# Performance work log

Hardware: AMD Instinct MI355X
Metric: run time of the kernel (lower is better)

The kernel has to match this reference:

```python
import jax, jax.numpy as jnp
import numpy as np
from jax import lax

WINDOW_SIZE = 11
NUM_SCALES = 4
SIGMA = 1.5
C1 = 0.01 ** 2
C2 = 0.03 ** 2
MS_WEIGHTS = (0.0448, 0.2856, 0.3001, 0.2363, 0.1333)


def _gaussian_window(window_size, sigma, channel, dtype):
    coords = jnp.arange(window_size, dtype=jnp.float32) - window_size // 2
    g = jnp.exp(-(coords ** 2) / (2.0 * sigma ** 2))
    g = g / g.sum()
    w2d = jnp.outer(g, g)  # [ws, ws]
    # depthwise kernel: [C, 1, ws, ws] (OIHW with feature_group_count=C)
    return jnp.broadcast_to(w2d, (channel, 1, window_size, window_size)).astype(dtype)


def _depthwise_conv(x, window, pad):
    C = x.shape[1]
    return lax.conv_general_dilated(
        x, window, window_strides=(1, 1), padding=[(pad, pad), (pad, pad)],
        dimension_numbers=('NCHW', 'OIHW', 'NCHW'), feature_group_count=C)


def _avg_pool2(x):
    s = lax.reduce_window(x, jnp.array(0.0, x.dtype), lax.add,
                          (1, 1, 2, 2), (1, 1, 2, 2), 'VALID')
    return s * jnp.asarray(0.25, x.dtype)


def _ssim_single_scale(img1, img2, window):
    pad = WINDOW_SIZE // 2
    mu1 = _depthwise_conv(img1, window, pad)
    mu2 = _depthwise_conv(img2, window, pad)
    mu1_sq = mu1 * mu1
    mu2_sq = mu2 * mu2
    mu1_mu2 = mu1 * mu2
    sigma1_sq = _depthwise_conv(img1 * img1, window, pad) - mu1_sq
    sigma2_sq = _depthwise_conv(img2 * img2, window, pad) - mu2_sq
    sigma12 = _depthwise_conv(img1 * img2, window, pad) - mu1_mu2
    ssim_map = ((2 * mu1_mu2 + C1) * (2 * sigma12 + C2)) / \
               ((mu1_sq + mu2_sq + C1) * (sigma1_sq + sigma2_sq + C2))
    return ssim_map.mean()  # size_average=True


def setup_inputs() -> dict:
    key = jax.random.key(0)
    k1, k2 = jax.random.split(key)
    shape = (16, 3, 512, 512)
    img1 = jax.random.uniform(k1, shape, dtype=jnp.float32)
    img2 = jax.random.uniform(k2, shape, dtype=jnp.float32)
    return {"img1": img1, "img2": img2}


def reference(img1, img2):
    channel = img1.shape[1]
    window = _gaussian_window(WINDOW_SIZE, SIGMA, channel, img1.dtype)
    loss = jnp.asarray(0.0, img1.dtype)
    x1, x2 = img1, img2
    for scale in range(NUM_SCALES):
        if scale > 0:
            x1 = _avg_pool2(x1)
            x2 = _avg_pool2(x2)
        ssim_val = _ssim_single_scale(x1, x2, window)
        w = MS_WEIGHTS[scale] if scale < len(MS_WEIGHTS) else 1.0 / NUM_SCALES
        loss = loss + w * (1.0 - ssim_val)
    return loss
```

## Files before the change

### kernel.cpp

```cpp
#include <hip/hip_runtime.h>

typedef float f2 __attribute__((ext_vector_type(2)));
typedef float f4 __attribute__((ext_vector_type(4)));

#define PAD 5
#define WSZ 11

__device__ __forceinline__ float gw(int k) {
    const float G[WSZ] = {
        0.0010283782f, 0.0075987580f, 0.0360007600f, 0.1093607000f,
        0.2130055600f, 0.2660117400f,
        0.2130055600f, 0.1093607000f, 0.0360007600f, 0.0075987580f, 0.0010283782f };
    return G[k];
}

__global__ __launch_bounds__(64) void pyramid_kernel(
    const float* __restrict__ img1, const float* __restrict__ img2,
    f2* __restrict__ p1, f2* __restrict__ p2, f2* __restrict__ p3)
{
    const int lane = threadIdx.x;
    const int cb = blockIdx.x;
    const int rb = blockIdx.y;
    const int z  = blockIdx.z;

    const size_t ibase = (size_t)z * 262144 + (size_t)(rb * 8) * 512 + cb * 256 + lane * 4;
    const float* b1 = img1 + ibase;
    const float* b2 = img2 + ibase;

    f4 A[8], B[8];
#pragma unroll
    for (int r = 0; r < 8; ++r) {
        A[r] = *(const f4*)(b1 + r * 512);
        B[r] = *(const f4*)(b2 + r * 512);
    }

    f2 u0, u1;
#pragma unroll
    for (int q = 0; q < 2; ++q) {
        f2 acc = {0.f, 0.f};
#pragma unroll
        for (int h = 0; h < 2; ++h) {
            const int rp = q * 2 + h;
            f4 a0 = A[2 * rp], a1 = A[2 * rp + 1];
            f4 c0 = B[2 * rp], c1 = B[2 * rp + 1];
            f2 v0 = { (a0.x + a0.y + a1.x + a1.y) * 0.25f,
                      (c0.x + c0.y + c1.x + c1.y) * 0.25f };
            f2 v1 = { (a0.z + a0.w + a1.z + a1.w) * 0.25f,
                      (c0.z + c0.w + c1.z + c1.w) * 0.25f };
            *(f4*)(p1 + (size_t)z * 65536 + (size_t)(rb * 4 + rp) * 256
                       + cb * 128 + lane * 2) = (f4){ v0.x, v0.y, v1.x, v1.y };
            acc += v0 + v1;
        }
        f2 u = acc * 0.25f;
        p2[(size_t)z * 16384 + (size_t)(rb * 2 + q) * 128 + cb * 64 + lane] = u;
        if (q == 0) u0 = u; else u1 = u;
    }
    f2 t = u0 + u1;
    t.x += __shfl_xor(t.x, 1);
    t.y += __shfl_xor(t.y, 1);
    if ((lane & 1) == 0)
        p3[(size_t)z * 4096 + (size_t)rb * 64 + cb * 32 + (lane >> 1)] = t * 0.25f;
}

template<int RT, bool PLANAR>
__device__ __forceinline__ float ssim_body(
    const float* __restrict__ img1, const float* __restrict__ img2,
    const f2* __restrict__ pair,
    int H, int W, int bx, int sy, int z, f2* st, int lane)
{
    const int ox = bx * 64;
    const int r0 = sy * RT;
    const size_t base = (size_t)z * H * W;

    constexpr int NIT  = RT + 10;
    constexpr int NIT2 = NIT / 2;
    const float C1 = 1e-4f, C2 = 9e-4f;

    const int c0 = ox - PAD + lane;
    const bool m0 = (c0 >= 0) & (c0 < W);
    const int c0c = min(max(c0, 0), W - 1);
    const int c1 = ox + 59 + lane;
    const bool m1 = (lane < 10) & (c1 < W);
    const int c1c = min(c1, W - 1);

    f2 P0a0={0.f,0.f}, P0a1={0.f,0.f}, P0b0={0.f,0.f}, P0b1={0.f,0.f};
    f2 P1a0={0.f,0.f}, P1a1={0.f,0.f}, P1b0={0.f,0.f}, P1b1={0.f,0.f};

    auto issue2 = [&](int y, f2& A0, f2& A1, f2& B0, f2& B1) {
        const int ya = min(max(y, 0), H - 1);
        const int yb = min(max(y + 1, 0), H - 1);
        const size_t ra = base + (size_t)ya * W;
        const size_t rb = base + (size_t)yb * W;
        if (PLANAR) {
            A0 = (f2){ img1[ra + c0c], img2[ra + c0c] };
            A1 = (f2){ img1[rb + c0c], img2[rb + c0c] };
            if (lane < 10) {
                B0 = (f2){ img1[ra + c1c], img2[ra + c1c] };
                B1 = (f2){ img1[rb + c1c], img2[rb + c1c] };
            }
        } else {
            A0 = pair[ra + c0c];
            A1 = pair[rb + c0c];
            if (lane < 10) { B0 = pair[ra + c1c]; B1 = pair[rb + c1c]; }
        }
    };

    issue2(r0 - PAD + 0, P0a0, P0a1, P0b0, P0b1);
    issue2(r0 - PAD + 2, P1a0, P1a1, P1b0, P1b1);

    f2 rmu[12], rsq[12];
    float rxx[12];
    float local = 0.f;
    const f2 zero = {0.f, 0.f};
    f2* st0 = st;
    f2* st1 = st + 80;

#pragma clang loop unroll(disable)
    for (int q0 = 0; q0 < NIT2; q0 += 6) {
#pragma unroll
        for (int j2 = 0; j2 < 6; ++j2) {
            const int i2 = q0 + j2;
            if (i2 < NIT2) {
                const int it0 = 2 * i2;
                const int y0 = r0 - PAD + it0;
                const bool yok0 = (y0 >= 0) & (y0 < H);
                const bool yok1 = (y0 + 1 >= 0) & (y0 + 1 < H);

                f2& a0 = (j2 & 1) ? P1a0 : P0a0;
                f2& a1 = (j2 & 1) ? P1a1 : P0a1;
                f2& b0 = (j2 & 1) ? P1b0 : P0b0;
                f2& b1 = (j2 & 1) ? P1b1 : P0b1;
                f2 wa0 = (yok0 & m0) ? a0 : zero;
                f2 wa1 = (yok1 & m0) ? a1 : zero;
                f2 wb0 = (yok0 & m1) ? b0 : zero;
                f2 wb1 = (yok1 & m1) ? b1 : zero;
                issue2(y0 + 4, a0, a1, b0, b1);

                __builtin_amdgcn_fence(__ATOMIC_ACQ_REL, "wavefront");
                __builtin_amdgcn_wave_barrier();
                st0[lane] = wa0;
                st1[lane] = wa1;
                if (lane < 10) { st0[64 + lane] = wb0; st1[64 + lane] = wb1; }
                __builtin_amdgcn_fence(__ATOMIC_ACQ_REL, "wavefront");
                __builtin_amdgcn_wave_barrier();

                f2 hmu0 = zero, hsq0 = zero, hmu1 = zero, hsq1 = zero;
                float hxx0 = 0.f, hxx1 = 0.f;
#pragma unroll
                for (int k = 0; k < WSZ; ++k) {
                    const float g = gw(k);
                    f2 p0 = st0[lane + k];
                    f2 p1 = st1[lane + k];
                    hmu0 += p0 * g;  hsq0 += (p0 * p0) * g;  hxx0 += (p0.x * p0.y) * g;
                    hmu1 += p1 * g;  hsq1 += (p1 * p1) * g;  hxx1 += (p1.x * p1.y) * g;
                }
                const int sE = 2 * j2;
                const int sO = 2 * j2 + 1;
                rmu[sE] = hmu0; rsq[sE] = hsq0; rxx[sE] = hxx0;
                rmu[sO] = hmu1; rsq[sO] = hsq1; rxx[sO] = hxx1;

                if (it0 >= 10) {
                    f2 vmu0 = zero, vsq0 = zero, vmu1 = zero, vsq1 = zero;
                    float vxx0 = 0.f, vxx1 = 0.f;
#pragma unroll
                    for (int k = 0; k < WSZ; ++k) {
                        const float g = gw(k);
                        const int sA = (2 * j2 + 2 + k) % 12;
                        const int sB = (2 * j2 + 3 + k) % 12;
                        vmu0 += rmu[sA] * g; vsq0 += rsq[sA] * g; vxx0 += rxx[sA] * g;
                        vmu1 += rmu[sB] * g; vsq1 += rsq[sB] * g; vxx1 += rxx[sB] * g;
                    }
                    {
                        const float mu1 = vmu0.x, mu2 = vmu0.y;
                        const float mu11 = mu1 * mu1, mu22 = mu2 * mu2, mu12 = mu1 * mu2;
                        const float sig1 = vsq0.x - mu11;
                        const float sig2 = vsq0.y - mu22;
                        const float sig12 = vxx0 - mu12;
                        const float num = (2.f * mu12 + C1) * (2.f * sig12 + C2);
                        const float den = (mu11 + mu22 + C1) * (sig1 + sig2 + C2);
                        local += num * __builtin_amdgcn_rcpf(den);
                    }
                    {
                        const float mu1 = vmu1.x, mu2 = vmu1.y;
                        const float mu11 = mu1 * mu1, mu22 = mu2 * mu2, mu12 = mu1 * mu2;
                        const float sig1 = vsq1.x - mu11;
                        const float sig2 = vsq1.y - mu22;
                        const float sig12 = vxx1 - mu12;
                        const float num = (2.f * mu12 + C1) * (2.f * sig12 + C2);
                        const float den = (mu11 + mu22 + C1) * (sig1 + sig2 + C2);
                        local += num * __builtin_amdgcn_rcpf(den);
                    }
                }
            }
        }
    }

#pragma unroll
    for (int off = 32; off > 0; off >>= 1) local += __shfl_down(local, off);
    return local;
}

__global__ __launch_bounds__(256, 2) void ssim_fused_kernel(
    const float* __restrict__ img1, const float* __restrict__ img2,
    const f2* __restrict__ p1, const f2* __restrict__ p2, const f2* __restrict__ p3,
    double* __restrict__ partials)
{
    __shared__ f2 st_all[4][160];
    const int lane = threadIdx.x & 63;
    const int wv   = threadIdx.x >> 6;
    f2* st = st_all[wv];

    const int i = blockIdx.x;
    const int z = i / 29;
    const int r = i - z * 29;

    float local;
    if (r < 16) {
        local = ssim_body<64, true>(img1, img2, nullptr, 512, 512,
                                    r & 7, (r >> 3) * 4 + wv, z, st, lane);
    } else if (r < 24) {
        const int l = r - 16;
        local = ssim_body<32, false>(nullptr, nullptr, p1, 256, 256,
                                     l & 3, (l >> 2) * 4 + wv, z, st, lane);
    } else if (r < 28) {
        const int l = r - 24;
        local = ssim_body<16, false>(nullptr, nullptr, p2, 128, 128,
                                     l & 1, (l >> 1) * 4 + wv, z, st, lane);
    } else {
        local = ssim_body<16, false>(nullptr, nullptr, p3, 64, 64,
                                     0, wv, z, st, lane);
    }
    if (lane == 0) partials[(size_t)i * 4 + wv] = (double)local;
}

__global__ __launch_bounds__(256) void finalize_kernel(
    const double* __restrict__ partials, float* __restrict__ out, int nw,
    double c0, double c1, double c2, double c3)
{
    double s[4] = {0.0, 0.0, 0.0, 0.0};
    for (int idx = threadIdx.x; idx < nw; idx += 256) {
        const int b = idx >> 2;
        const int g = b / 29;
        const int r = b - g * 29;
        const int sc = (r < 16) ? 0 : (r < 24) ? 1 : (r < 28) ? 2 : 3;
        s[sc] += partials[idx];
    }
    __shared__ double sm[4][256];
    sm[0][threadIdx.x] = s[0]; sm[1][threadIdx.x] = s[1];
    sm[2][threadIdx.x] = s[2]; sm[3][threadIdx.x] = s[3];
    __syncthreads();
    if (threadIdx.x == 0) {
        const double w[4] = {0.0448, 0.2856, 0.3001, 0.2363};
        const double cnt[4] = {c0, c1, c2, c3};
        double loss = 0.0;
#pragma unroll
        for (int sc = 0; sc < 4; ++sc) {
            double t = 0.0;
            for (int k = 0; k < 256; ++k) t += sm[sc][k];
            loss += w[sc] * (1.0 - t / cnt[sc]);
        }
        out[0] = (float)loss;
    }
}

extern "C" void kernel_launch(void* const* d_in, const int* in_sizes, int n_in,
                              void* d_out, int out_size, void* d_ws, size_t ws_size,
                              hipStream_t stream) {
    const float* img1 = (const float*)d_in[0];
    const float* img2 = (const float*)d_in[1];
    float* out = (float*)d_out;

    const int H0 = 512, W0 = 512;
    const int NC = in_sizes[0] / (H0 * W0);

    double* partials = (double*)d_ws;
    f2* p1 = (f2*)((char*)d_ws + 65536);
    f2* p2 = p1 + (size_t)NC * 256 * 256;
    f2* p3 = p2 + (size_t)NC * 128 * 128;

    pyramid_kernel<<<dim3(2, 64, NC), 64, 0, stream>>>(img1, img2, p1, p2, p3);

    const int NBLK = NC * 29;
    ssim_fused_kernel<<<dim3(NBLK), 256, 0, stream>>>(img1, img2, p1, p2, p3, partials);

    const double c0 = (double)NC * 512.0 * 512.0;
    const double c1 = (double)NC * 256.0 * 256.0;
    const double c2 = (double)NC * 128.0 * 128.0;
    const double c3 = (double)NC * 64.0 * 64.0;
    finalize_kernel<<<1, 256, 0, stream>>>(partials, out, NBLK * 4, c0, c1, c2, c3);
}
```

Measured before the change: 236.4 us.

## Fuse pyramid into SSIM kernel with atomic dependency counter

Folds the pyramid downsampling kernel into the fused SSIM kernel as leading blocks. Scale-0 SSIM blocks, which need only the original images, run concurrently with pyramid construction. Blocks for the coarser scales spin on an agent-scope atomic counter until all pyramid blocks have finished. This removes a kernel launch boundary and lets the pyramid work overlap with full-resolution SSIM. It relies on pyramid blocks being scheduled before the waiting blocks to avoid deadlock, and adds a memset call.

New measurement: 301.4 us. 27.5% more time.

```diff
diff --git a/kernel.cpp b/kernel.cpp
--- a/kernel.cpp
+++ b/kernel.cpp
@@ -14,15 +14,11 @@
     return G[k];
 }
 
-__global__ __launch_bounds__(64) void pyramid_kernel(
+__device__ __forceinline__ void pyramid_unit(
     const float* __restrict__ img1, const float* __restrict__ img2,
-    f2* __restrict__ p1, f2* __restrict__ p2, f2* __restrict__ p3)
+    f2* __restrict__ p1, f2* __restrict__ p2, f2* __restrict__ p3,
+    int cb, int rb, int z, int lane)
 {
-    const int lane = threadIdx.x;
-    const int cb = blockIdx.x;
-    const int rb = blockIdx.y;
-    const int z  = blockIdx.z;
-
     const size_t ibase = (size_t)z * 262144 + (size_t)(rb * 8) * 512 + cb * 256 + lane * 4;
     const float* b1 = img1 + ibase;
     const float* b2 = img2 + ibase;
@@ -202,47 +198,82 @@
 
 __global__ __launch_bounds__(256, 2) void ssim_fused_kernel(
     const float* __restrict__ img1, const float* __restrict__ img2,
-    const f2* __restrict__ p1, const f2* __restrict__ p2, const f2* __restrict__ p3,
+    f2* __restrict__ p1, f2* __restrict__ p2, f2* __restrict__ p3,
+    unsigned* __restrict__ done, int npb, int ns0,
     double* __restrict__ partials)
 {
     __shared__ f2 st_all[4][160];
     const int lane = threadIdx.x & 63;
     const int wv   = threadIdx.x >> 6;
+
+    const int i = blockIdx.x;
+
+    if (i < npb) {
+#pragma unroll
+        for (int ii = 0; ii < 4; ++ii) {
+            const int u = (i * 4 + wv) * 4 + ii;
+            pyramid_unit(img1, img2, p1, p2, p3,
+                         u & 1, (u >> 1) & 63, u >> 7, lane);
+        }
+        __threadfence();
+        __syncthreads();
+        if (threadIdx.x == 0)
+            __hip_atomic_fetch_add(done, 1u, __ATOMIC_RELEASE,
+                                   __HIP_MEMORY_SCOPE_AGENT);
+        return;
+    }
+
+    const int j = i - npb;
     f2* st = st_all[wv];
-
-    const int i = blockIdx.x;
-    const int z = i / 29;
-    const int r = i - z * 29;
-
     float local;
-    if (r < 16) {
+
+    if (j < ns0) {
+        const int z = j >> 4, r = j & 15;
         local = ssim_body<64, true>(img1, img2, nullptr, 512, 512,
                                     r & 7, (r >> 3) * 4 + wv, z, st, lane);
-    } else if (r < 24) {
-        const int l = r - 16;
-        local = ssim_body<32, false>(nullptr, nullptr, p1, 256, 256,
-                                     l & 3, (l >> 2) * 4 + wv, z, st, lane);
-    } else if (r < 28) {
-        const int l = r - 24;
-        local = ssim_body<16, false>(nullptr, nullptr, p2, 128, 128,
-                                     l & 1, (l >> 1) * 4 + wv, z, st, lane);
     } else {
-        local = ssim_body<16, false>(nullptr, nullptr, p3, 64, 64,
-                                     0, wv, z, st, lane);
-    }
-    if (lane == 0) partials[(size_t)i * 4 + wv] = (double)local;
+        if (threadIdx.x == 0) {
+            while (__hip_atomic_load(done, __ATOMIC_ACQUIRE,
+                                     __HIP_MEMORY_SCOPE_AGENT) < (unsigned)npb)
+                __builtin_amdgcn_s_sleep(64);
+        }
+        __syncthreads();
+        __builtin_amdgcn_fence(__ATOMIC_ACQUIRE, "agent");
+
+        const int c = j - ns0;
+        const int z = c / 13;
+        const int r = c - z * 13;
+        if (r < 8) {
+            local = ssim_body<32, false>(nullptr, nullptr, p1, 256, 256,
+                                         r & 3, (r >> 2) * 4 + wv, z, st, lane);
+        } else if (r < 12) {
+            const int l = r - 8;
+            local = ssim_body<16, false>(nullptr, nullptr, p2, 128, 128,
+                                         l & 1, (l >> 1) * 4 + wv, z, st, lane);
+        } else {
+            local = ssim_body<16, false>(nullptr, nullptr, p3, 64, 64,
+                                         0, wv, z, st, lane);
+        }
+    }
+    if (lane == 0) partials[(size_t)j * 4 + wv] = (double)local;
 }
 
 __global__ __launch_bounds__(256) void finalize_kernel(
-    const double* __restrict__ partials, float* __restrict__ out, int nw,
+    const double* __restrict__ partials, float* __restrict__ out,
+    int nw, int ns0,
     double c0, double c1, double c2, double c3)
 {
     double s[4] = {0.0, 0.0, 0.0, 0.0};
     for (int idx = threadIdx.x; idx < nw; idx += 256) {
         const int b = idx >> 2;
-        const int g = b / 29;
-        const int r = b - g * 29;
-        const int sc = (r < 16) ? 0 : (r < 24) ? 1 : (r < 28) ? 2 : 3;
+        int sc;
+        if (b < ns0) sc = 0;
+        else {
+            const int c = b - ns0;
+            const int z = c / 13;
+            const int r = c - z * 13;
+            sc = (r < 8) ? 1 : (r < 12) ? 2 : 3;
+        }
         s[sc] += partials[idx];
     }
     __shared__ double sm[4][256];
@@ -273,19 +304,24 @@
     const int H0 = 512, W0 = 512;
     const int NC = in_sizes[0] / (H0 * W0);
 
-    double* partials = (double*)d_ws;
+    unsigned* done = (unsigned*)d_ws;
+    double* partials = (double*)((char*)d_ws + 64);
     f2* p1 = (f2*)((char*)d_ws + 65536);
     f2* p2 = p1 + (size_t)NC * 256 * 256;
     f2* p3 = p2 + (size_t)NC * 128 * 128;
 
-    pyramid_kernel<<<dim3(2, 64, NC), 64, 0, stream>>>(img1, img2, p1, p2, p3);
-
-    const int NBLK = NC * 29;
-    ssim_fused_kernel<<<dim3(NBLK), 256, 0, stream>>>(img1, img2, p1, p2, p3, partials);
+    hipMemsetAsync(done, 0, sizeof(unsigned), stream);
+
+    const int NPB = NC * 8;
+    const int NS0 = NC * 16;
+    const int NBLK = NPB + NS0 + NC * 13;
+    ssim_fused_kernel<<<dim3(NBLK), 256, 0, stream>>>(
+        img1, img2, p1, p2, p3, done, NPB, NS0, partials);
 
     const double c0 = (double)NC * 512.0 * 512.0;
     const double c1 = (double)NC * 256.0 * 256.0;
     const double c2 = (double)NC * 128.0 * 128.0;
     const double c3 = (double)NC * 64.0 * 64.0;
-    finalize_kernel<<<1, 256, 0, stream>>>(partials, out, NBLK * 4, c0, c1, c2, c3);
-}
+    finalize_kernel<<<1, 256, 0, stream>>>(partials, out, (NS0 + NC * 13) * 4,
+                                           NS0, c0, c1, c2, c3);
+}
```

## Fuse pyramid downsampling into SSIM kernel, computing pooled pixels on the fly

Applied to the files above, without the earlier changes.

Removes the separate pyramid kernel and its intermediate buffers. The coarser-scale SSIM paths now read the original images and average 2x2, 4x4 or 8x8 blocks inline while loading each row. This saves one kernel launch and the write and re-read of the pooled images. In exchange it re-reads full-resolution data for the coarse scales, with many more loads per pooled pixel (up to 128 floats at the coarsest scale), adds more code paths, and can raise register pressure.

Result: slower. 320.5 us (+35.6%).

```diff
diff --git a/kernel.cpp b/kernel.cpp
--- a/kernel.cpp
+++ b/kernel.cpp
@@ -14,63 +14,15 @@
     return G[k];
 }
 
-__global__ __launch_bounds__(64) void pyramid_kernel(
+template<int RT>
+__device__ __forceinline__ float ssim_body2(
     const float* __restrict__ img1, const float* __restrict__ img2,
-    f2* __restrict__ p1, f2* __restrict__ p2, f2* __restrict__ p3)
+    int bx, int sy, int z, f2* st, int lane)
 {
-    const int lane = threadIdx.x;
-    const int cb = blockIdx.x;
-    const int rb = blockIdx.y;
-    const int z  = blockIdx.z;
-
-    const size_t ibase = (size_t)z * 262144 + (size_t)(rb * 8) * 512 + cb * 256 + lane * 4;
-    const float* b1 = img1 + ibase;
-    const float* b2 = img2 + ibase;
-
-    f4 A[8], B[8];
-#pragma unroll
-    for (int r = 0; r < 8; ++r) {
-        A[r] = *(const f4*)(b1 + r * 512);
-        B[r] = *(const f4*)(b2 + r * 512);
-    }
-
-    f2 u0, u1;
-#pragma unroll
-    for (int q = 0; q < 2; ++q) {
-        f2 acc = {0.f, 0.f};
-#pragma unroll
-        for (int h = 0; h < 2; ++h) {
-            const int rp = q * 2 + h;
-            f4 a0 = A[2 * rp], a1 = A[2 * rp + 1];
-            f4 c0 = B[2 * rp], c1 = B[2 * rp + 1];
-            f2 v0 = { (a0.x + a0.y + a1.x + a1.y) * 0.25f,
-                      (c0.x + c0.y + c1.x + c1.y) * 0.25f };
-            f2 v1 = { (a0.z + a0.w + a1.z + a1.w) * 0.25f,
-                      (c0.z + c0.w + c1.z + c1.w) * 0.25f };
-            *(f4*)(p1 + (size_t)z * 65536 + (size_t)(rb * 4 + rp) * 256
-                       + cb * 128 + lane * 2) = (f4){ v0.x, v0.y, v1.x, v1.y };
-            acc += v0 + v1;
-        }
-        f2 u = acc * 0.25f;
-        p2[(size_t)z * 16384 + (size_t)(rb * 2 + q) * 128 + cb * 64 + lane] = u;
-        if (q == 0) u0 = u; else u1 = u;
-    }
-    f2 t = u0 + u1;
-    t.x += __shfl_xor(t.x, 1);
-    t.y += __shfl_xor(t.y, 1);
-    if ((lane & 1) == 0)
-        p3[(size_t)z * 4096 + (size_t)rb * 64 + cb * 32 + (lane >> 1)] = t * 0.25f;
-}
-
-template<int RT, bool PLANAR>
-__device__ __forceinline__ float ssim_body(
-    const float* __restrict__ img1, const float* __restrict__ img2,
-    const f2* __restrict__ pair,
-    int H, int W, int bx, int sy, int z, f2* st, int lane)
-{
+    const int H = 512, W = 512;
     const int ox = bx * 64;
     const int r0 = sy * RT;
-    const size_t base = (size_t)z * H * W;
+    const size_t base = (size_t)z * 262144;
 
     constexpr int NIT  = RT + 10;
     constexpr int NIT2 = NIT / 2;
@@ -91,17 +43,11 @@
         const int yb = min(max(y + 1, 0), H - 1);
         const size_t ra = base + (size_t)ya * W;
         const size_t rb = base + (size_t)yb * W;
-        if (PLANAR) {
-            A0 = (f2){ img1[ra + c0c], img2[ra + c0c] };
-            A1 = (f2){ img1[rb + c0c], img2[rb + c0c] };
-            if (lane < 10) {
-                B0 = (f2){ img1[ra + c1c], img2[ra + c1c] };
-                B1 = (f2){ img1[rb + c1c], img2[rb + c1c] };
-            }
-        } else {
-            A0 = pair[ra + c0c];
-            A1 = pair[rb + c0c];
-            if (lane < 10) { B0 = pair[ra + c1c]; B1 = pair[rb + c1c]; }
+        A0 = (f2){ img1[ra + c0c], img2[ra + c0c] };
+        A1 = (f2){ img1[rb + c0c], img2[rb + c0c] };
+        if (lane < 10) {
+            B0 = (f2){ img1[ra + c1c], img2[ra + c1c] };
+            B1 = (f2){ img1[rb + c1c], img2[rb + c1c] };
         }
     };
 
@@ -200,9 +146,163 @@
     return local;
 }
 
+template<int RT, int F>
+__device__ __forceinline__ float ssim_body1(
+    const float* __restrict__ img1, const float* __restrict__ img2,
+    int bx, int sy, int z, f2* st, int lane)
+{
+    constexpr int W = 512 / F, H = 512 / F;
+    const int ox = bx * 64;
+    const int r0 = sy * RT;
+    const size_t base = (size_t)z * 262144;
+    constexpr int NIT = RT + 10;
+    const float C1 = 1e-4f, C2 = 9e-4f;
+
+    const int c0 = ox - PAD + lane;
+    const bool m0 = (c0 >= 0) & (c0 < W);
+    const int c0c = min(max(c0, 0), W - 1);
+    const int c1 = ox + 59 + lane;
+    const bool m1 = (lane < 10) & (c1 < W);
+    const int c1c = min(c1, W - 1);
+
+    const f2 zero = {0.f, 0.f};
+
+    f2 P0a[4], P0b[4], P1a[4], P1b[4];
+#pragma unroll
+    for (int k = 0; k < 4; ++k) { P0a[k]=zero; P0b[k]=zero; P1a[k]=zero; P1b[k]=zero; }
+
+    auto issueP = [&](int y, f2* A, f2* B) {
+        const int yc = min(max(y, 0), H - 1);
+        const float* q1 = img1 + base + (size_t)(2 * yc) * 512;
+        const float* q2 = img2 + base + (size_t)(2 * yc) * 512;
+        A[0] = *(const f2*)(q1 + 2 * c0c);
+        A[1] = *(const f2*)(q1 + 512 + 2 * c0c);
+        A[2] = *(const f2*)(q2 + 2 * c0c);
+        A[3] = *(const f2*)(q2 + 512 + 2 * c0c);
+        if (lane < 10) {
+            B[0] = *(const f2*)(q1 + 2 * c1c);
+            B[1] = *(const f2*)(q1 + 512 + 2 * c1c);
+            B[2] = *(const f2*)(q2 + 2 * c1c);
+            B[3] = *(const f2*)(q2 + 512 + 2 * c1c);
+        }
+    };
+    auto pool2v = [](const f2* A) -> f2 {
+        return (f2){ (A[0].x + A[0].y + A[1].x + A[1].y) * 0.25f,
+                     (A[2].x + A[2].y + A[3].x + A[3].y) * 0.25f };
+    };
+    auto loadPool = [&](int yc, int cc) -> f2 {
+        if constexpr (F == 4) {
+            float sa = 0.f, sb = 0.f;
+#pragma unroll
+            for (int rr = 0; rr < 4; ++rr) {
+                f4 a = *(const f4*)(img1 + base + (size_t)(4 * yc + rr) * 512 + 4 * cc);
+                f4 b = *(const f4*)(img2 + base + (size_t)(4 * yc + rr) * 512 + 4 * cc);
+                sa += (a.x + a.y) + (a.z + a.w);
+                sb += (b.x + b.y) + (b.z + b.w);
+            }
+            return (f2){ sa * 0.0625f, sb * 0.0625f };
+        } else {
+            float sa = 0.f, sb = 0.f;
+#pragma unroll
+            for (int rr = 0; rr < 8; ++rr) {
+                const float* q1 = img1 + base + (size_t)(8 * yc + rr) * 512 + 8 * cc;
+                const float* q2 = img2 + base + (size_t)(8 * yc + rr) * 512 + 8 * cc;
+                f4 a0 = *(const f4*)(q1);  f4 a1 = *(const f4*)(q1 + 4);
+                f4 b0 = *(const f4*)(q2);  f4 b1 = *(const f4*)(q2 + 4);
+                sa += (a0.x + a0.y + a0.z + a0.w) + (a1.x + a1.y + a1.z + a1.w);
+                sb += (b0.x + b0.y + b0.z + b0.w) + (b1.x + b1.y + b1.z + b1.w);
+            }
+            return (f2){ sa * (1.f / 64.f), sb * (1.f / 64.f) };
+        }
+    };
+
+    if constexpr (F == 2) {
+        issueP(r0 - PAD + 0, P0a, P0b);
+        issueP(r0 - PAD + 1, P1a, P1b);
+    }
+
+    f2 rmu[12], rsq[12];
+    float rxx[12];
+    float local = 0.f;
+
+#pragma clang loop unroll(disable)
+    for (int b0 = 0; b0 < NIT; b0 += 12) {
+#pragma unroll
+        for (int j = 0; j < 12; ++j) {
+            const int it = b0 + j;
+            if (it < NIT) {
+                const int y = r0 - PAD + it;
+                const bool yok = (y >= 0) & (y < H);
+
+                f2 wa, wb = zero;
+                if constexpr (F == 2) {
+                    f2* A = (j & 1) ? P1a : P0a;
+                    f2* B = (j & 1) ? P1b : P0b;
+                    f2 pa = pool2v(A);
+                    f2 pb = pool2v(B);
+                    wa = (yok & m0) ? pa : zero;
+                    wb = (yok & m1) ? pb : zero;
+                    issueP(y + 2, A, B);
+                } else {
+                    const int yc = min(max(y, 0), H - 1);
+                    f2 pa = loadPool(yc, c0c);
+                    wa = (yok & m0) ? pa : zero;
+                    if (lane < 10) {
+                        f2 pb = loadPool(yc, c1c);
+                        wb = (yok & m1) ? pb : zero;
+                    }
+                }
+
+                __builtin_amdgcn_fence(__ATOMIC_ACQ_REL, "wavefront");
+                __builtin_amdgcn_wave_barrier();
+                st[lane] = wa;
+                if (lane < 10) st[64 + lane] = wb;
+                __builtin_amdgcn_fence(__ATOMIC_ACQ_REL, "wavefront");
+                __builtin_amdgcn_wave_barrier();
+
+                f2 hmu = zero, hsq = zero;
+                float hxx = 0.f;
+#pragma unroll
+                for (int k = 0; k < WSZ; ++k) {
+                    f2 p = st[lane + k];
+                    hmu += p * gw(k);
+                    hsq += (p * p) * gw(k);
+                    hxx += (p.x * p.y) * gw(k);
+                }
+                rmu[it % 12] = hmu;
+                rsq[it % 12] = hsq;
+                rxx[it % 12] = hxx;
+
+                if (it >= 10) {
+                    f2 vmu = zero, vsq = zero;
+                    float vxx = 0.f;
+#pragma unroll
+                    for (int k = 0; k < WSZ; ++k) {
+                        const int s = (j + 2 + k) % 12;
+                        vmu += rmu[s] * gw(k);
+                        vsq += rsq[s] * gw(k);
+                        vxx += rxx[s] * gw(k);
+                    }
+                    const float mu1 = vmu.x, mu2 = vmu.y;
+                    const float mu11 = mu1 * mu1, mu22 = mu2 * mu2, mu12 = mu1 * mu2;
+                    const float sig1 = vsq.x - mu11;
+                    const float sig2 = vsq.y - mu22;
+                    const float sig12 = vxx - mu12;
+                    const float num = (2.f * mu12 + C1) * (2.f * sig12 + C2);
+                    const float den = (mu11 + mu22 + C1) * (sig1 + sig2 + C2);
+                    local += num * __builtin_amdgcn_rcpf(den);
+                }
+            }
+        }
+    }
+
+#pragma unroll
+    for (int off = 32; off > 0; off >>= 1) local += __shfl_down(local, off);
+    return local;
+}
+
 __global__ __launch_bounds__(256, 2) void ssim_fused_kernel(
     const float* __restrict__ img1, const float* __restrict__ img2,
-    const f2* __restrict__ p1, const f2* __restrict__ p2, const f2* __restrict__ p3,
     double* __restrict__ partials)
 {
     __shared__ f2 st_all[4][160];
@@ -216,19 +316,15 @@
 
     float local;
     if (r < 16) {
-        local = ssim_body<64, true>(img1, img2, nullptr, 512, 512,
-                                    r & 7, (r >> 3) * 4 + wv, z, st, lane);
+        local = ssim_body2<64>(img1, img2, r & 7, (r >> 3) * 4 + wv, z, st, lane);
     } else if (r < 24) {
         const int l = r - 16;
-        local = ssim_body<32, false>(nullptr, nullptr, p1, 256, 256,
-                                     l & 3, (l >> 2) * 4 + wv, z, st, lane);
+        local = ssim_body1<32, 2>(img1, img2, l & 3, (l >> 2) * 4 + wv, z, st, lane);
     } else if (r < 28) {
         const int l = r - 24;
-        local = ssim_body<16, false>(nullptr, nullptr, p2, 128, 128,
-                                     l & 1, (l >> 1) * 4 + wv, z, st, lane);
+        local = ssim_body1<16, 4>(img1, img2, l & 1, (l >> 1) * 4 + wv, z, st, lane);
     } else {
-        local = ssim_body<16, false>(nullptr, nullptr, p3, 64, 64,
-                                     0, wv, z, st, lane);
+        local = ssim_body1<16, 8>(img1, img2, 0, wv, z, st, lane);
     }
     if (lane == 0) partials[(size_t)i * 4 + wv] = (double)local;
 }
@@ -274,14 +370,9 @@
     const int NC = in_sizes[0] / (H0 * W0);
 
     double* partials = (double*)d_ws;
-    f2* p1 = (f2*)((char*)d_ws + 65536);
-    f2* p2 = p1 + (size_t)NC * 256 * 256;
-    f2* p3 = p2 + (size_t)NC * 128 * 128;
-
-    pyramid_kernel<<<dim3(2, 64, NC), 64, 0, stream>>>(img1, img2, p1, p2, p3);
 
     const int NBLK = NC * 29;
-    ssim_fused_kernel<<<dim3(NBLK), 256, 0, stream>>>(img1, img2, p1, p2, p3, partials);
+    ssim_fused_kernel<<<dim3(NBLK), 256, 0, stream>>>(img1, img2, partials);
 
     const double c0 = (double)NC * 512.0 * 512.0;
     const double c1 = (double)NC * 256.0 * 256.0;
```
